# Performance work log

Measured on AMD Instinct MI355X. Metric: run time of the kernel, lower is better.

Reference implementation:

```python
import jax, jax.numpy as jnp
import numpy as np

N = 2048
K = 10000
MEAN = 1.0
CHUNK = 8  # rows per scan step; intermediate is CHUNK x N x K (~655 MB)


def setup_inputs() -> dict:
    key = jax.random.key(0)
    # torch.rand(N, 10000) * mean / 2
    W = jax.random.uniform(key, (N, K), dtype=jnp.float32) * (MEAN / 2.0)
    return {"W": W}


def reference(W):
    # H[i, j] = max_k ( |W[i,k]| + |W[j,k]| )  -- tropical (max-plus) gram matrix
    A = jnp.abs(W)                     # (N, K)
    n, k = A.shape
    chunks = A.reshape(n // CHUNK, CHUNK, k)

    @jax.checkpoint
    def body(carry, a):                # a: (CHUNK, K)
        # (CHUNK, N, K) broadcast-add, max-reduce over K -> (CHUNK, N)
        h = jnp.max(a[:, None, :] + A[None, :, :], axis=-1)
        return carry, h

    _, H = jax.lax.scan(body, None, chunks)  # (n//CHUNK, CHUNK, N)
    return H.reshape(n, n)
```

## Files before the change

kernel.cpp:

```cpp
#include <hip/hip_runtime.h>
#include <math.h>


constexpr int N  = 2048;
constexpr int K  = 10000;
constexpr int BT = 128;
constexpr int BK = 32;
constexpr int NT = N / BT;
constexpr int NTRI = NT * (NT + 1) / 2;
constexpr int TILES8 = 72;
constexpr int BID8 = TILES8 * 8;
constexpr int CH8 = 1252;
constexpr int CH7 = 1432;
constexpr int NS8 = 40;
constexpr int NS7 = 45;
constexpr int PAD = 132;
constexpr size_t WT_BYTES = (size_t)K * N * sizeof(float);

typedef float f32x2 __attribute__((ext_vector_type(2)));

__device__ __forceinline__ float max3f(float a, float b, float c) {
    float d;
    asm("v_max3_f32 %0, %1, %2, %3" : "=v"(d) : "v"(a), "v"(b), "v"(c));
    return d;
}

__global__ void zero_out_kernel(float4* __restrict__ p, int n4) {
    const int i = blockIdx.x * blockDim.x + threadIdx.x;
    if (i < n4) p[i] = make_float4(0.f, 0.f, 0.f, 0.f);
}

__global__ __launch_bounds__(256)
void transpose_abs_kernel(const float* __restrict__ W, float* __restrict__ WT) {
    __shared__ float S[64][65];
    const int i0 = blockIdx.x * 64;
    const int k0 = blockIdx.y * 64;
    const int tid = threadIdx.x;
#pragma unroll
    for (int w = 0; w < 16; ++w) {
        const int idx = w * 256 + tid;
        const int r = idx >> 6, c = idx & 63;
        if (k0 + c < K) S[r][c] = fabsf(W[(size_t)(i0 + r) * K + k0 + c]);
    }
    __syncthreads();
#pragma unroll
    for (int w = 0; w < 16; ++w) {
        const int idx = w * 256 + tid;
        const int r = idx >> 6, c = idx & 63;
        if (k0 + r < K) WT[(size_t)(k0 + r) * N + i0 + c] = S[c][r];
    }
}

__global__ __launch_bounds__(256, 2)
void gram_wt_kernel(const float* __restrict__ WT, float* __restrict__ H) {
    __shared__ float As[BK][PAD];

    const int tid = threadIdx.x;

    const int bid = blockIdx.x;
    int tile, kbeg, nstep;
    if (bid < BID8) {
        tile  = bid >> 3;
        kbeg  = (bid & 7) * CH8;
        nstep = NS8;
    } else {
        const int r = bid - BID8;
        tile  = TILES8 + r / 7;
        kbeg  = (r % 7) * CH7;
        nstep = NS7;
    }
    int t = tile;
    int bi = 0;
    while (t >= NT - bi) { t -= NT - bi; ++bi; }
    const int bj = bi + t;
    const int i0 = bi * BT, j0 = bj * BT;

    const int skk  = tid >> 3;
    const int soff = (tid & 7) * 16;

    const int tx = tid & 15, ty = tid >> 4;
    const int ra = ty * 4, rb = ra + 64;
    const int ca = tx * 4, cb = ca + 64;

    float acc[8][8];
#pragma unroll
    for (int m = 0; m < 8; ++m)
#pragma unroll
        for (int n = 0; n < 8; ++n) acc[m][n] = 0.0f;

    float4 va[4];
    auto fetchA = [&](int s) {
        int kg = kbeg + s * BK + skk;
        if (kg > K - 1) kg = K - 1;
        const float* src = WT + (size_t)kg * N + i0 + soff;
#pragma unroll
        for (int q = 0; q < 4; ++q)
            va[q] = *reinterpret_cast<const float4*>(src + q * 4);
    };

    const float* __restrict__ bAp = WT + j0 + ca;
    const float* __restrict__ bBp = WT + j0 + cb;
    float4 b[4][4];
    auto fetchB = [&](int buf, int kg) {
        const int k0c = kg     > K - 1 ? K - 1 : kg;
        const int k1c = kg + 1 > K - 1 ? K - 1 : kg + 1;
        b[buf][0] = *reinterpret_cast<const float4*>(bAp + (size_t)k0c * N);
        b[buf][1] = *reinterpret_cast<const float4*>(bBp + (size_t)k0c * N);
        b[buf][2] = *reinterpret_cast<const float4*>(bAp + (size_t)k1c * N);
        b[buf][3] = *reinterpret_cast<const float4*>(bBp + (size_t)k1c * N);
    };

    fetchA(0);
    fetchB(0, kbeg);
    fetchB(1, kbeg + 2);

    for (int s = 0; s < nstep; ++s) {
        asm volatile("s_barrier" ::: "memory");
#pragma unroll
        for (int q = 0; q < 4; ++q)
            *reinterpret_cast<float4*>(&As[skk][soff + q * 4]) = va[q];
        if (s + 1 < nstep) fetchA(s + 1);
        asm volatile("s_waitcnt lgkmcnt(0)\n\ts_barrier" ::: "memory");

        const int kgs = kbeg + s * BK;
#pragma unroll
        for (int p = 0; p < 16; ++p) {
            fetchB((p + 2) & 3, kgs + 2 * p + 4);

            const int kk = 2 * p;
            const float4 A0a = *reinterpret_cast<const float4*>(&As[kk][ra]);
            const float4 A0b = *reinterpret_cast<const float4*>(&As[kk][rb]);
            const float4 A1a = *reinterpret_cast<const float4*>(&As[kk + 1][ra]);
            const float4 A1b = *reinterpret_cast<const float4*>(&As[kk + 1][rb]);
            const float a0[8] = {A0a.x, A0a.y, A0a.z, A0a.w, A0b.x, A0b.y, A0b.z, A0b.w};
            const float a1[8] = {A1a.x, A1a.y, A1a.z, A1a.w, A1b.x, A1b.y, A1b.z, A1b.w};
            const float4 c0 = b[p & 3][0], c1 = b[p & 3][1];
            const float4 c2 = b[p & 3][2], c3 = b[p & 3][3];
            const f32x2 b0p[4] = {{c0.x, c0.y}, {c0.z, c0.w}, {c1.x, c1.y}, {c1.z, c1.w}};
            const f32x2 b1p[4] = {{c2.x, c2.y}, {c2.z, c2.w}, {c3.x, c3.y}, {c3.z, c3.w}};
#pragma unroll
            for (int m = 0; m < 8; ++m) {
                const f32x2 am0 = {a0[m], a0[m]};
                const f32x2 am1 = {a1[m], a1[m]};
#pragma unroll
                for (int np = 0; np < 4; ++np) {
                    const f32x2 t0 = am0 + b0p[np];
                    const f32x2 t1 = am1 + b1p[np];
                    acc[m][2 * np]     = max3f(acc[m][2 * np],     t0.x, t1.x);
                    acc[m][2 * np + 1] = max3f(acc[m][2 * np + 1], t0.y, t1.y);
                }
            }
        }
    }

    int* Hi = (int*)H;
#pragma unroll
    for (int m = 0; m < 8; ++m) {
        const int r = (m < 4) ? (ra + m) : (rb + m - 4);
#pragma unroll
        for (int n = 0; n < 8; ++n) {
            const int c = (n < 4) ? (ca + n) : (cb + n - 4);
            atomicMax(&Hi[(size_t)(i0 + r) * N + j0 + c], __float_as_int(acc[m][n]));
        }
    }
}

__global__ __launch_bounds__(256, 2)
void tropical_gram_kernel(const float* __restrict__ W, float* __restrict__ H) {
    __shared__ float As[BK][BT];
    __shared__ float Bs[BK][BT];
    const int tid = threadIdx.x;
    const int bid = blockIdx.x;
    int tile, kbeg, nstep;
    if (bid < BID8) { tile = bid >> 3; kbeg = (bid & 7) * CH8; nstep = NS8; }
    else { const int r = bid - BID8; tile = TILES8 + r / 7; kbeg = (r % 7) * CH7; nstep = NS7; }
    int t = tile; int bi = 0;
    while (t >= NT - bi) { t -= NT - bi; ++bi; }
    const int bj = bi + t;
    const int i0 = bi * BT, j0 = bj * BT;
    const bool diag = (bi == bj);
    const int srow = tid & 127, kh = tid >> 7;
    const float* rowi = W + (size_t)(i0 + srow) * K + kbeg + kh * 16;
    const float* rowj = W + (size_t)(j0 + srow) * K + kbeg + kh * 16;
    const int tx = tid & 15, ty = tid >> 4;
    const int ra = ty * 4, rb = ra + 64, ca = tx * 4, cb = ca + 64;
    float acc[8][8];
#pragma unroll
    for (int m = 0; m < 8; ++m)
#pragma unroll
        for (int n = 0; n < 8; ++n) acc[m][n] = 0.0f;
    float4 va[4], vb[4];
    const float4 z4 = make_float4(0.f, 0.f, 0.f, 0.f);
    auto fetchA = [&](int s) {
#pragma unroll
        for (int qq = 0; qq < 4; ++qq) {
            const int kg = kbeg + kh * 16 + s * BK + qq * 4;
            va[qq] = (kg < K) ? *reinterpret_cast<const float4*>(rowi + s * BK + qq * 4) : z4;
        }
    };
    auto fetchB = [&](int s) {
#pragma unroll
        for (int qq = 0; qq < 4; ++qq) {
            const int kg = kbeg + kh * 16 + s * BK + qq * 4;
            vb[qq] = (kg < K) ? *reinterpret_cast<const float4*>(rowj + s * BK + qq * 4) : z4;
        }
    };
    fetchA(0);
    if (!diag) fetchB(0);
    const float (*Bsrc)[BT] = diag ? As : Bs;
    for (int s = 0; s < nstep; ++s) {
        __syncthreads();
#pragma unroll
        for (int qq = 0; qq < 4; ++qq) {
            const int kb = kh * 16 + qq * 4;
            As[kb + 0][srow] = fabsf(va[qq].x);
            As[kb + 1][srow] = fabsf(va[qq].y);
            As[kb + 2][srow] = fabsf(va[qq].z);
            As[kb + 3][srow] = fabsf(va[qq].w);
        }
        if (!diag) {
#pragma unroll
            for (int qq = 0; qq < 4; ++qq) {
                const int kb = kh * 16 + qq * 4;
                Bs[kb + 0][srow] = fabsf(vb[qq].x);
                Bs[kb + 1][srow] = fabsf(vb[qq].y);
                Bs[kb + 2][srow] = fabsf(vb[qq].z);
                Bs[kb + 3][srow] = fabsf(vb[qq].w);
            }
        }
        if (s + 1 < nstep) { fetchA(s + 1); if (!diag) fetchB(s + 1); }
        __syncthreads();
#pragma unroll 2
        for (int kk = 0; kk < BK; kk += 2) {
            const float4 A0a = *reinterpret_cast<const float4*>(&As[kk][ra]);
            const float4 A0b = *reinterpret_cast<const float4*>(&As[kk][rb]);
            const float4 A1a = *reinterpret_cast<const float4*>(&As[kk + 1][ra]);
            const float4 A1b = *reinterpret_cast<const float4*>(&As[kk + 1][rb]);
            const float4 B0a = *reinterpret_cast<const float4*>(&Bsrc[kk][ca]);
            const float4 B0b = *reinterpret_cast<const float4*>(&Bsrc[kk][cb]);
            const float4 B1a = *reinterpret_cast<const float4*>(&Bsrc[kk + 1][ca]);
            const float4 B1b = *reinterpret_cast<const float4*>(&Bsrc[kk + 1][cb]);
            const float a0[8] = {A0a.x, A0a.y, A0a.z, A0a.w, A0b.x, A0b.y, A0b.z, A0b.w};
            const float a1[8] = {A1a.x, A1a.y, A1a.z, A1a.w, A1b.x, A1b.y, A1b.z, A1b.w};
            const float b0[8] = {B0a.x, B0a.y, B0a.z, B0a.w, B0b.x, B0b.y, B0b.z, B0b.w};
            const float b1[8] = {B1a.x, B1a.y, B1a.z, B1a.w, B1b.x, B1b.y, B1b.z, B1b.w};
#pragma unroll
            for (int m = 0; m < 8; ++m)
#pragma unroll
                for (int n = 0; n < 8; ++n)
                    acc[m][n] = max3f(acc[m][n], a0[m] + b0[n], a1[m] + b1[n]);
        }
    }
    int* Hi = (int*)H;
#pragma unroll
    for (int m = 0; m < 8; ++m) {
        const int r = (m < 4) ? (ra + m) : (rb + m - 4);
#pragma unroll
        for (int n = 0; n < 8; ++n) {
            const int c = (n < 4) ? (ca + n) : (cb + n - 4);
            atomicMax(&Hi[(size_t)(i0 + r) * N + j0 + c], __float_as_int(acc[m][n]));
        }
    }
}

constexpr int MT = 64;
constexpr int NT64 = N / MT;
constexpr int NMIR = NT64 * (NT64 - 1) / 2;

__global__ __launch_bounds__(256)
void mirror_kernel(float* __restrict__ H) {
    __shared__ float S[MT][MT + 1];
    int t = blockIdx.x;
    int ti = 0;
    while (t >= NT64 - 1 - ti) { t -= NT64 - 1 - ti; ++ti; }
    const int tj = ti + 1 + t;
    const int r0 = ti * MT, c0 = tj * MT;
    const int tid = threadIdx.x;
#pragma unroll
    for (int w = 0; w < 16; ++w) {
        const int idx = w * 256 + tid;
        const int r = idx >> 6, c = idx & 63;
        S[r][c] = H[(size_t)(r0 + r) * N + c0 + c];
    }
    __syncthreads();
#pragma unroll
    for (int w = 0; w < 16; ++w) {
        const int idx = w * 256 + tid;
        const int r = idx >> 6, c = idx & 63;
        H[(size_t)(c0 + r) * N + r0 + c] = S[c][r];
    }
}

extern "C" void kernel_launch(void* const* d_in, const int* in_sizes, int n_in,
                              void* d_out, int out_size, void* d_ws, size_t ws_size,
                              hipStream_t stream) {
    const float* W = (const float*)d_in[0];
    float* H = (float*)d_out;
    (void)in_sizes; (void)n_in; (void)out_size;

    const int n4 = N * N / 4;
    zero_out_kernel<<<(n4 + 255) / 256, 256, 0, stream>>>((float4*)H, n4);

    if (ws_size >= WT_BYTES) {
        float* WT = (float*)d_ws;
        transpose_abs_kernel<<<dim3(N / 64, (K + 63) / 64), dim3(256), 0, stream>>>(W, WT);
        gram_wt_kernel<<<dim3(1024), dim3(256), 0, stream>>>(WT, H);
    } else {
        tropical_gram_kernel<<<dim3(1024), dim3(256), 0, stream>>>(W, H);
    }
    mirror_kernel<<<dim3(NMIR), dim3(256), 0, stream>>>(H);
}
```

Before: 1.013 ms.

## Stage A/B tiles into LDS via global_load_lds with double buffering

Replaces the gram kernel's register-staged A tile and direct-from-global B loads with a double-buffered LDS pipeline. Both operands are copied straight into shared memory with the global_load_lds builtin, and the K step drops to 16. Diagonal tiles reuse the A buffer instead of loading B, which skips redundant traffic. The fallback kernel also gets lighter barriers and packed float2 adds, but it only runs when the workspace is too small. The new path adds a barrier every 16 k-steps and relies on the async LDS copy finishing by the __syncthreads, which is an ordering risk.

New measurement: 921.4 us. 9.1% less time.

```diff
diff --git a/kernel.cpp b/kernel.cpp
--- a/kernel.cpp
+++ b/kernel.cpp
@@ -5,16 +5,18 @@
 constexpr int N  = 2048;
 constexpr int K  = 10000;
 constexpr int BT = 128;
+constexpr int BKD = 16;
 constexpr int BK = 32;
 constexpr int NT = N / BT;
-constexpr int NTRI = NT * (NT + 1) / 2;
 constexpr int TILES8 = 72;
 constexpr int BID8 = TILES8 * 8;
 constexpr int CH8 = 1252;
 constexpr int CH7 = 1432;
+constexpr int NSD8 = 79;
+constexpr int NSD7 = 90;
 constexpr int NS8 = 40;
 constexpr int NS7 = 45;
-constexpr int PAD = 132;
+
 constexpr size_t WT_BYTES = (size_t)K * N * sizeof(float);
 
 typedef float f32x2 __attribute__((ext_vector_type(2)));
@@ -23,6 +25,13 @@
     float d;
     asm("v_max3_f32 %0, %1, %2, %3" : "=v"(d) : "v"(a), "v"(b), "v"(c));
     return d;
+}
+
+__device__ __forceinline__ void gload16(const void* g, void* l) {
+    __builtin_amdgcn_global_load_lds(
+        (const __attribute__((address_space(1))) void*)g,
+        (__attribute__((address_space(3))) void*)l,
+        16, 0, 0);
 }
 
 __global__ void zero_out_kernel(float4* __restrict__ p, int n4) {
@@ -52,31 +61,35 @@
 }
 
 __global__ __launch_bounds__(256, 2)
-void gram_wt_kernel(const float* __restrict__ WT, float* __restrict__ H) {
-    __shared__ float As[BK][PAD];
-
-    const int tid = threadIdx.x;
+void gram_dma_kernel(const float* __restrict__ WT, float* __restrict__ H) {
+    __shared__ float As[2][BKD][BT];
+    __shared__ float Bs[2][BKD][BT];
+
+    const int tid  = threadIdx.x;
+    const int lane = tid & 63;
+    const int wid  = tid >> 6;
 
     const int bid = blockIdx.x;
     int tile, kbeg, nstep;
     if (bid < BID8) {
         tile  = bid >> 3;
         kbeg  = (bid & 7) * CH8;
-        nstep = NS8;
+        nstep = NSD8;
     } else {
         const int r = bid - BID8;
         tile  = TILES8 + r / 7;
         kbeg  = (r % 7) * CH7;
-        nstep = NS7;
+        nstep = NSD7;
     }
     int t = tile;
     int bi = 0;
     while (t >= NT - bi) { t -= NT - bi; ++bi; }
     const int bj = bi + t;
     const int i0 = bi * BT, j0 = bj * BT;
-
-    const int skk  = tid >> 3;
-    const int soff = (tid & 7) * 16;
+    const bool diag = (bi == bj);
+
+    const int krow_off = lane >> 5;
+    const int i_off    = (lane & 31) * 4;
 
     const int tx = tid & 15, ty = tid >> 4;
     const int ra = ty * 4, rb = ra + 64;
@@ -88,56 +101,52 @@
 #pragma unroll
         for (int n = 0; n < 8; ++n) acc[m][n] = 0.0f;
 
-    float4 va[4];
-    auto fetchA = [&](int s) {
-        int kg = kbeg + s * BK + skk;
-        if (kg > K - 1) kg = K - 1;
-        const float* src = WT + (size_t)kg * N + i0 + soff;
-#pragma unroll
-        for (int q = 0; q < 4; ++q)
-            va[q] = *reinterpret_cast<const float4*>(src + q * 4);
+    auto stage = [&](int nb, int s) {
+        const int kbase = kbeg + s * BKD;
+#pragma unroll
+        for (int q = 0; q < 2; ++q) {
+            const int cc = wid * 2 + q;
+            int k = kbase + 2 * cc + krow_off;
+            if (k > K - 1) k = K - 1;
+            gload16(WT + (size_t)k * N + i0 + i_off,
+                    (char*)&As[nb][0][0] + cc * 1024);
+        }
+        if (!diag) {
+#pragma unroll
+            for (int q = 0; q < 2; ++q) {
+                const int cc = wid * 2 + q;
+                int k = kbase + 2 * cc + krow_off;
+                if (k > K - 1) k = K - 1;
+                gload16(WT + (size_t)k * N + j0 + i_off,
+                        (char*)&Bs[nb][0][0] + cc * 1024);
+            }
+        }
     };
 
-    const float* __restrict__ bAp = WT + j0 + ca;
-    const float* __restrict__ bBp = WT + j0 + cb;
-    float4 b[4][4];
-    auto fetchB = [&](int buf, int kg) {
-        const int k0c = kg     > K - 1 ? K - 1 : kg;
-        const int k1c = kg + 1 > K - 1 ? K - 1 : kg + 1;
-        b[buf][0] = *reinterpret_cast<const float4*>(bAp + (size_t)k0c * N);
-        b[buf][1] = *reinterpret_cast<const float4*>(bBp + (size_t)k0c * N);
-        b[buf][2] = *reinterpret_cast<const float4*>(bAp + (size_t)k1c * N);
-        b[buf][3] = *reinterpret_cast<const float4*>(bBp + (size_t)k1c * N);
-    };
-
-    fetchA(0);
-    fetchB(0, kbeg);
-    fetchB(1, kbeg + 2);
+    stage(0, 0);
+    __syncthreads();
 
     for (int s = 0; s < nstep; ++s) {
-        asm volatile("s_barrier" ::: "memory");
-#pragma unroll
-        for (int q = 0; q < 4; ++q)
-            *reinterpret_cast<float4*>(&As[skk][soff + q * 4]) = va[q];
-        if (s + 1 < nstep) fetchA(s + 1);
-        asm volatile("s_waitcnt lgkmcnt(0)\n\ts_barrier" ::: "memory");
-
-        const int kgs = kbeg + s * BK;
-#pragma unroll
-        for (int p = 0; p < 16; ++p) {
-            fetchB((p + 2) & 3, kgs + 2 * p + 4);
-
-            const int kk = 2 * p;
-            const float4 A0a = *reinterpret_cast<const float4*>(&As[kk][ra]);
-            const float4 A0b = *reinterpret_cast<const float4*>(&As[kk][rb]);
-            const float4 A1a = *reinterpret_cast<const float4*>(&As[kk + 1][ra]);
-            const float4 A1b = *reinterpret_cast<const float4*>(&As[kk + 1][rb]);
+        const int cur = s & 1;
+        if (s + 1 < nstep) stage(cur ^ 1, s + 1);
+
+        const float (*Acur)[BT] = As[cur];
+        const float (*Bcur)[BT] = diag ? As[cur] : Bs[cur];
+
+#pragma unroll 2
+        for (int kk = 0; kk < BKD; kk += 2) {
+            const float4 A0a = *reinterpret_cast<const float4*>(&Acur[kk][ra]);
+            const float4 A0b = *reinterpret_cast<const float4*>(&Acur[kk][rb]);
+            const float4 A1a = *reinterpret_cast<const float4*>(&Acur[kk + 1][ra]);
+            const float4 A1b = *reinterpret_cast<const float4*>(&Acur[kk + 1][rb]);
+            const float4 B0a = *reinterpret_cast<const float4*>(&Bcur[kk][ca]);
+            const float4 B0b = *reinterpret_cast<const float4*>(&Bcur[kk][cb]);
+            const float4 B1a = *reinterpret_cast<const float4*>(&Bcur[kk + 1][ca]);
+            const float4 B1b = *reinterpret_cast<const float4*>(&Bcur[kk + 1][cb]);
             const float a0[8] = {A0a.x, A0a.y, A0a.z, A0a.w, A0b.x, A0b.y, A0b.z, A0b.w};
             const float a1[8] = {A1a.x, A1a.y, A1a.z, A1a.w, A1b.x, A1b.y, A1b.z, A1b.w};
-            const float4 c0 = b[p & 3][0], c1 = b[p & 3][1];
-            const float4 c2 = b[p & 3][2], c3 = b[p & 3][3];
-            const f32x2 b0p[4] = {{c0.x, c0.y}, {c0.z, c0.w}, {c1.x, c1.y}, {c1.z, c1.w}};
-            const f32x2 b1p[4] = {{c2.x, c2.y}, {c2.z, c2.w}, {c3.x, c3.y}, {c3.z, c3.w}};
+            const f32x2 b0p[4] = {{B0a.x, B0a.y}, {B0a.z, B0a.w}, {B0b.x, B0b.y}, {B0b.z, B0b.w}};
+            const f32x2 b1p[4] = {{B1a.x, B1a.y}, {B1a.z, B1a.w}, {B1b.x, B1b.y}, {B1b.z, B1b.w}};
 #pragma unroll
             for (int m = 0; m < 8; ++m) {
                 const f32x2 am0 = {a0[m], a0[m]};
@@ -151,6 +160,7 @@
                 }
             }
         }
+        __syncthreads();
     }
 
     int* Hi = (int*)H;
@@ -209,7 +219,7 @@
     if (!diag) fetchB(0);
     const float (*Bsrc)[BT] = diag ? As : Bs;
     for (int s = 0; s < nstep; ++s) {
-        __syncthreads();
+        asm volatile("s_barrier" ::: "memory");
 #pragma unroll
         for (int qq = 0; qq < 4; ++qq) {
             const int kb = kh * 16 + qq * 4;
@@ -229,7 +239,7 @@
             }
         }
         if (s + 1 < nstep) { fetchA(s + 1); if (!diag) fetchB(s + 1); }
-        __syncthreads();
+        asm volatile("s_waitcnt lgkmcnt(0)\n\ts_barrier" ::: "memory");
 #pragma unroll 2
         for (int kk = 0; kk < BK; kk += 2) {
             const float4 A0a = *reinterpret_cast<const float4*>(&As[kk][ra]);
@@ -242,13 +252,20 @@
             const float4 B1b = *reinterpret_cast<const float4*>(&Bsrc[kk + 1][cb]);
             const float a0[8] = {A0a.x, A0a.y, A0a.z, A0a.w, A0b.x, A0b.y, A0b.z, A0b.w};
             const float a1[8] = {A1a.x, A1a.y, A1a.z, A1a.w, A1b.x, A1b.y, A1b.z, A1b.w};
-            const float b0[8] = {B0a.x, B0a.y, B0a.z, B0a.w, B0b.x, B0b.y, B0b.z, B0b.w};
-            const float b1[8] = {B1a.x, B1a.y, B1a.z, B1a.w, B1b.x, B1b.y, B1b.z, B1b.w};
-#pragma unroll
-            for (int m = 0; m < 8; ++m)
-#pragma unroll
-                for (int n = 0; n < 8; ++n)
-                    acc[m][n] = max3f(acc[m][n], a0[m] + b0[n], a1[m] + b1[n]);
+            const f32x2 b0p[4] = {{B0a.x, B0a.y}, {B0a.z, B0a.w}, {B0b.x, B0b.y}, {B0b.z, B0b.w}};
+            const f32x2 b1p[4] = {{B1a.x, B1a.y}, {B1a.z, B1a.w}, {B1b.x, B1b.y}, {B1b.z, B1b.w}};
+#pragma unroll
+            for (int m = 0; m < 8; ++m) {
+                const f32x2 am0 = {a0[m], a0[m]};
+                const f32x2 am1 = {a1[m], a1[m]};
+#pragma unroll
+                for (int np = 0; np < 4; ++np) {
+                    const f32x2 t0 = am0 + b0p[np];
+                    const f32x2 t1 = am1 + b1p[np];
+                    acc[m][2 * np]     = max3f(acc[m][2 * np],     t0.x, t1.x);
+                    acc[m][2 * np + 1] = max3f(acc[m][2 * np + 1], t0.y, t1.y);
+                }
+            }
         }
     }
     int* Hi = (int*)H;
@@ -304,7 +321,7 @@
     if (ws_size >= WT_BYTES) {
         float* WT = (float*)d_ws;
         transpose_abs_kernel<<<dim3(N / 64, (K + 63) / 64), dim3(256), 0, stream>>>(W, WT);
-        gram_wt_kernel<<<dim3(1024), dim3(256), 0, stream>>>(WT, H);
+        gram_dma_kernel<<<dim3(1024), dim3(256), 0, stream>>>(WT, H);
     } else {
         tropical_gram_kernel<<<dim3(1024), dim3(256), 0, stream>>>(W, H);
     }
```
